# Kernel optimization log

Hardware: AMD Instinct MI355X
Metric: run time of the kernel (lower is better)

Reference implementation:

```python
import jax, jax.numpy as jnp
import numpy as np

DIM = 768
DEPTH = 12
HEADS = 12
DIM_HEAD = DIM // HEADS
DIM_MLP = 3072
PATCH = 16
SPECTRA = 4096
NUM_PATCHES = SPECTRA // PATCH
NUM_CLASSES = 1000
SCALE = DIM_HEAD ** -0.5
EPS = 1e-5


def sincos_pos_embed(embed_dim, n_pos):
    omega = np.arange(embed_dim // 2, dtype=np.float64) / (embed_dim / 2.0)
    omega = 1.0 / 10000 ** omega
    pos = np.arange(n_pos, dtype=np.float64)
    out = np.einsum('m,d->md', pos, omega)
    emb = np.concatenate([np.sin(out), np.cos(out)], axis=1)
    emb = np.concatenate([np.zeros([1, embed_dim]), emb], axis=0)  # cls slot
    return jnp.asarray(emb, jnp.float32)  # [N+1, D]


def setup_inputs() -> dict:
    key = jax.random.key(0)
    ks = jax.random.split(key, 12)
    s = 0.02
    d = {
        'x': jax.random.normal(ks[0], (32, 1, SPECTRA), jnp.float32),
        'conv_w': jax.random.normal(ks[1], (PATCH, DIM), jnp.float32) * s,
        'conv_b': jnp.zeros((DIM,), jnp.float32),
        'pos_embed': sincos_pos_embed(DIM, NUM_PATCHES),
        'cls_token': jax.random.normal(ks[2], (1, DIM), jnp.float32) * s,
        'ln1_w': jnp.ones((DEPTH, DIM), jnp.float32),
        'ln1_b': jnp.zeros((DEPTH, DIM), jnp.float32),
        'qkv_w': jax.random.normal(ks[3], (DEPTH, DIM, 3 * DIM), jnp.float32) * s,
        'out_w': jax.random.normal(ks[4], (DEPTH, DIM, DIM), jnp.float32) * s,
        'out_b': jnp.zeros((DEPTH, DIM), jnp.float32),
        'ln2_w': jnp.ones((DEPTH, DIM), jnp.float32),
        'ln2_b': jnp.zeros((DEPTH, DIM), jnp.float32),
        'mlp_w1': jax.random.normal(ks[5], (DEPTH, DIM, DIM_MLP), jnp.float32) * s,
        'mlp_b1': jnp.zeros((DEPTH, DIM_MLP), jnp.float32),
        'mlp_w2': jax.random.normal(ks[6], (DEPTH, DIM_MLP, DIM), jnp.float32) * s,
        'mlp_b2': jnp.zeros((DEPTH, DIM), jnp.float32),
        'cls_ln_w': jnp.ones((DIM,), jnp.float32),
        'cls_ln_b': jnp.zeros((DIM,), jnp.float32),
        'head_w': jax.random.normal(ks[7], (DIM, NUM_CLASSES), jnp.float32) * s,
        'head_b': jnp.zeros((NUM_CLASSES,), jnp.float32),
    }
    return d


def _ln(z, w, b):
    mu = z.mean(-1, keepdims=True)
    var = ((z - mu) ** 2).mean(-1, keepdims=True)
    return (z - mu) / jnp.sqrt(var + EPS) * w + b


def _forward(x, conv_w, conv_b, pos_embed, cls_token,
             ln1_w, ln1_b, qkv_w, out_w, out_b, ln2_w, ln2_b,
             mlp_w1, mlp_b1, mlp_w2, mlp_b2,
             cls_ln_w, cls_ln_b, head_w, head_b):
    B = x.shape[0]
    # Conv1d(1, D, k=P, stride=P) == non-overlapping patch linear proj
    patches = x.reshape(B, NUM_PATCHES, PATCH)
    h = patches @ conv_w + conv_b                         # [B, N, D]
    h = h + pos_embed[1:]
    cls = cls_token + pos_embed[:1]                       # [1, D]
    h = jnp.concatenate([jnp.broadcast_to(cls[None], (B, 1, DIM)), h], axis=1)  # [B, N+1, D]

    def block(h, p):
        l1w, l1b, qw, ow, ob, l2w, l2b, w1, b1, w2, b2 = p
        skip = h
        z = _ln(h, l1w, l1b)
        qkv = z @ qw                                      # [B, n, 3D]
        q, k, v = jnp.split(qkv, 3, axis=-1)
        def heads(t):
            return t.reshape(B, -1, HEADS, DIM_HEAD).transpose(0, 2, 1, 3)
        q, k, v = heads(q), heads(k), heads(v)            # [B, H, n, dh]
        dots = jnp.einsum('bhid,bhjd->bhij', q, k) * SCALE
        attn = jax.nn.softmax(dots, axis=-1)
        o = jnp.einsum('bhij,bhjd->bhid', attn, v)
        o = o.transpose(0, 2, 1, 3).reshape(B, -1, DIM)
        h = o @ ow + ob + skip
        skip = h
        z = _ln(h, l2w, l2b)
        z = jax.nn.gelu(z @ w1 + b1, approximate=False) @ w2 + b2
        return z + skip, None

    params = (ln1_w, ln1_b, qkv_w, out_w, out_b, ln2_w, ln2_b,
              mlp_w1, mlp_b1, mlp_w2, mlp_b2)
    h, _ = jax.lax.scan(block, h, params)
    cls_out = _ln(h[:, 0], cls_ln_w, cls_ln_b)
    return cls_out @ head_w + head_b                      # [B, num_classes]


def reference(x, conv_w, conv_b, pos_embed, cls_token,
              ln1_w, ln1_b, qkv_w, out_w, out_b, ln2_w, ln2_b,
              mlp_w1, mlp_b1, mlp_w2, mlp_b2,
              cls_ln_w, cls_ln_b, head_w, head_b):
    return _forward(x, conv_w, conv_b, pos_embed, cls_token,
                    ln1_w, ln1_b, qkv_w, out_w, out_b, ln2_w, ln2_b,
                    mlp_w1, mlp_b1, mlp_w2, mlp_b2,
                    cls_ln_w, cls_ln_b, head_w, head_b)
```

## Files before the change

### kernel.cpp

```cpp
#include <hip/hip_runtime.h>
#include <math.h>

#define DIM 768
#define DEPTH 12
#define HEADS 12
#define DIM_HEAD 64
#define DIM_MLP 3072
#define PATCH 16
#define NUM_PATCHES 256
#define SEQ 257
#define NUM_CLASSES 1000
#define BATCH 32
#define SCALE 0.125f
#define EPS 1e-5f
#define ROWS 8224
#define PAD_ROWS 8320
#define PAD_A 8448

typedef short bf16x8 __attribute__((ext_vector_type(8)));
typedef float f32x4 __attribute__((ext_vector_type(4)));

__device__ inline unsigned short f2bf(float f) {
    union { float f; unsigned int u; } c; c.f = f;
    unsigned int u = c.u;
    return (unsigned short)((u + 0x7fffu + ((u >> 16) & 1u)) >> 16);
}

#define MFMA16(d, a, b) d = __builtin_amdgcn_mfma_f32_16x16x32_bf16(a, b, d, 0, 0, 0)
#define SBAR() asm volatile("s_barrier" ::: "memory")
#define LGKM0() asm volatile("s_waitcnt lgkmcnt(0)" ::: "memory")

__global__ void patch_embed_kernel(const float* __restrict__ x,
                                   const float* __restrict__ conv_w,
                                   const float* __restrict__ conv_b,
                                   const float* __restrict__ pos,
                                   const float* __restrict__ cls_tok,
                                   float* __restrict__ h) {
    int row = blockIdx.x;
    int b = row / SEQ;
    int r = row % SEQ;
    int t = threadIdx.x;
    float* out = h + (long)row * DIM;
    if (r == 0) {
        for (int d = t; d < DIM; d += 256)
            out[d] = cls_tok[d] + pos[d];
        return;
    }
    int p = r - 1;
    const float* xp = x + (long)b * 4096 + p * PATCH;
    float xv[PATCH];
#pragma unroll
    for (int k = 0; k < PATCH; ++k) xv[k] = xp[k];
    for (int d = t; d < DIM; d += 256) {
        float acc = conv_b[d];
#pragma unroll
        for (int k = 0; k < PATCH; ++k)
            acc += xv[k] * conv_w[k * DIM + d];
        out[d] = acc + pos[(long)r * DIM + d];
    }
}

template <int OBF>
__global__ void layernorm_kernel(const float* __restrict__ in, long in_stride,
                                 const float* __restrict__ w,
                                 const float* __restrict__ bia,
                                 void* __restrict__ out) {
    __shared__ float red[8];
    long row = blockIdx.x;
    const float* src = in + row * in_stride;
    int t = threadIdx.x;
    float v0 = src[t], v1 = src[t + 256], v2 = src[t + 512];
    float s = v0 + v1 + v2;
    float q = v0 * v0 + v1 * v1 + v2 * v2;
#pragma unroll
    for (int off = 32; off; off >>= 1) {
        s += __shfl_down(s, off);
        q += __shfl_down(q, off);
    }
    if ((t & 63) == 0) { red[t >> 6] = s; red[4 + (t >> 6)] = q; }
    __syncthreads();
    if (t == 0) {
        float ss = red[0] + red[1] + red[2] + red[3];
        float qq = red[4] + red[5] + red[6] + red[7];
        float mu = ss * (1.0f / DIM);
        float var = qq * (1.0f / DIM) - mu * mu;
        red[0] = mu;
        red[1] = rsqrtf(var + EPS);
    }
    __syncthreads();
    float mu = red[0], rstd = red[1];
    float o0 = (v0 - mu) * rstd * w[t] + bia[t];
    float o1 = (v1 - mu) * rstd * w[t + 256] + bia[t + 256];
    float o2 = (v2 - mu) * rstd * w[t + 512] + bia[t + 512];
    if (OBF) {
        unsigned short* dst = (unsigned short*)out + row * DIM;
        dst[t] = f2bf(o0); dst[t + 256] = f2bf(o1); dst[t + 512] = f2bf(o2);
    } else {
        float* dst = (float*)out + row * DIM;
        dst[t] = o0; dst[t + 256] = o1; dst[t + 512] = o2;
    }
}

__global__ void transpose_all_kernel(const float* __restrict__ qw,
                                     const float* __restrict__ ow,
                                     const float* __restrict__ w1,
                                     const float* __restrict__ w2,
                                     unsigned short* __restrict__ qwT,
                                     unsigned short* __restrict__ owT,
                                     unsigned short* __restrict__ w1T,
                                     unsigned short* __restrict__ w2T) {
    __shared__ float tile[32][33];
    int t = blockIdx.x;
    const float* src; unsigned short* dst; int K, N, kt, nt;
    if (t < 1728)      {            src = qw; dst = qwT; K = 768;  N = 2304; kt = t % 24; nt = t / 24; }
    else if (t < 2304) { t -= 1728; src = ow; dst = owT; K = 768;  N = 768;  kt = t % 24; nt = t / 24; }
    else if (t < 4608) { t -= 2304; src = w1; dst = w1T; K = 768;  N = 3072; kt = t % 24; nt = t / 24; }
    else               { t -= 4608; src = w2; dst = w2T; K = 3072; N = 768;  kt = t % 96; nt = t / 96; }
    int k0 = kt * 32, n0 = nt * 32;
    int c = threadIdx.x & 31, r0 = threadIdx.x >> 5;
#pragma unroll
    for (int rr = r0; rr < 32; rr += 8)
        tile[rr][c] = src[(long)(k0 + rr) * N + n0 + c];
    __syncthreads();
#pragma unroll
    for (int rr = r0; rr < 32; rr += 8)
        dst[(long)(n0 + rr) * K + k0 + c] = f2bf(tile[c][rr]);
}

__global__ __launch_bounds__(256) void attn_kernel(const unsigned short* __restrict__ qkv,
                                                   unsigned short* __restrict__ o) {
    __shared__ unsigned short sh[60416];
    const int tid = threadIdx.x;
    const int lane = tid & 63;
    const int w = tid >> 6;

    const int nwg = gridDim.x;
    const int orig = blockIdx.x;
    const int q = nwg >> 3, r = nwg & 7;
    const int xcd = orig & 7, idx = orig >> 3;
    const int wg = (xcd < r ? xcd * (q + 1) : r * (q + 1) + (xcd - r) * q) + idx;
    const int bh = wg / 5, qt = wg % 5;
    const int b = bh / HEADS, hh = bh % HEADS;
    const unsigned short* qbase = qkv + (long)b * SEQ * 2304 + hh * 64;
    const unsigned short* kbase = qbase + 768;
    const unsigned short* vbase = qbase + 1536;

#pragma unroll
    for (int u = 0; u < 2; ++u) {
        int c = tid + u * 256;
        int j = c >> 3, cb = c & 7;
        int gj = qt * 64 + j; if (gj > 256) gj = 256;
        const unsigned short* g = qbase + (long)gj * 2304 + ((cb ^ (j & 7)) << 3);
        __builtin_amdgcn_global_load_lds(
            (const __attribute__((address_space(1))) void*)g,
            (__attribute__((address_space(3))) void*)&sh[j * 64 + cb * 8], 16, 0, 0);
    }
#pragma unroll
    for (int u = 0; u < 9; ++u) {
        int c = tid + u * 256;
        int j = c >> 3, cb = c & 7;
        int gj = j > 256 ? 256 : j;
        const unsigned short* g = kbase + (long)gj * 2304 + ((cb ^ (j & 7)) << 3);
        __builtin_amdgcn_global_load_lds(
            (const __attribute__((address_space(1))) void*)g,
            (__attribute__((address_space(3))) void*)&sh[4096 + j * 64 + cb * 8], 16, 0, 0);
    }
#pragma unroll
    for (int u = 0; u < 9; ++u) {
        int c = tid + u * 256;
        int j = c >> 3, dc = c & 7;
        short vv[8] = {0, 0, 0, 0, 0, 0, 0, 0};
        if (j < SEQ) *(bf16x8*)vv = *(const bf16x8*)(vbase + (long)j * 2304 + dc * 8);
#pragma unroll
        for (int e = 0; e < 8; ++e)
            sh[22528 + (dc * 8 + e) * 296 + j] = (unsigned short)vv[e];
    }
    __syncthreads();

    f32x4 s[18] = {};
#pragma unroll
    for (int ks = 0; ks < 2; ++ks) {
        int arow = w * 16 + (lane & 15);
        int cb = ks * 4 + (lane >> 4);
        bf16x8 aq = *(const bf16x8*)&sh[arow * 64 + ((cb ^ (arow & 7)) << 3)];
#pragma unroll
        for (int nf = 0; nf < 18; ++nf) {
            int brow = nf * 16 + (lane & 15);
            bf16x8 bk = *(const bf16x8*)&sh[4096 + brow * 64 + ((cb ^ (brow & 7)) << 3)];
            MFMA16(s[nf], aq, bk);
        }
    }

    float inv[4];
#pragma unroll
    for (int j = 0; j < 4; ++j) {
        float m_ = -3.0e38f;
#pragma unroll
        for (int nf = 0; nf < 18; ++nf) {
            int col = nf * 16 + (lane & 15);
            float x = (col < SEQ) ? s[nf][j] * SCALE : -3.0e38f;
            s[nf][j] = x;
            m_ = fmaxf(m_, x);
        }
#pragma unroll
        for (int off = 1; off < 16; off <<= 1) m_ = fmaxf(m_, __shfl_xor(m_, off));
        float sm = 0.f;
#pragma unroll
        for (int nf = 0; nf < 18; ++nf) {
            float e = __expf(s[nf][j] - m_);
            s[nf][j] = e;
            sm += e;
        }
#pragma unroll
        for (int off = 1; off < 16; off <<= 1) sm += __shfl_xor(sm, off);
        inv[j] = 1.0f / sm;
    }
#pragma unroll
    for (int nf = 0; nf < 18; ++nf) {
        int col = nf * 16 + (lane & 15);
#pragma unroll
        for (int j = 0; j < 4; ++j) {
            int row = w * 16 + (lane >> 4) * 4 + j;
            sh[41472 + row * 296 + col] = f2bf(s[nf][j] * inv[j]);
        }
    }
    __syncthreads();

    f32x4 oa[4] = {};
#pragma unroll
    for (int ks = 0; ks < 9; ++ks) {
        int prow = w * 16 + (lane & 15);
        bf16x8 ap = *(const bf16x8*)&sh[41472 + prow * 296 + ks * 32 + (lane >> 4) * 8];
#pragma unroll
        for (int n = 0; n < 4; ++n) {
            int drow = n * 16 + (lane & 15);
            bf16x8 bv = *(const bf16x8*)&sh[22528 + drow * 296 + ks * 32 + (lane >> 4) * 8];
            MFMA16(oa[n], ap, bv);
        }
    }
#pragma unroll
    for (int n = 0; n < 4; ++n) {
        int col = hh * 64 + n * 16 + (lane & 15);
#pragma unroll
        for (int j = 0; j < 4; ++j) {
            int gr = qt * 64 + w * 16 + (lane >> 4) * 4 + j;
            if (gr < SEQ)
                o[((long)(b * SEQ + gr)) * DIM + col] = f2bf(oa[n][j]);
        }
    }
}

template <int NK, int ACT>
__global__ __launch_bounds__(512, 2) void gemm256_kernel(
    const unsigned short* __restrict__ A,
    const unsigned short* __restrict__ Bt,
    const float* __restrict__ bias,
    unsigned short* __restrict__ C,
    int M, int GY, int lda, int ldb, int ldc) {
    __shared__ unsigned short sh[65536];
    const int tid = threadIdx.x;
    const int lane = tid & 63;
    const int w = tid >> 6;
    const int wr = w >> 2;
    const int wn = w & 3;

    const int nwg = gridDim.x;
    const int orig = blockIdx.x;
    const int q = nwg >> 3, r = nwg & 7;
    const int xcd = orig & 7, idx = orig >> 3;
    const int wg = (xcd < r ? xcd * (q + 1) : r * (q + 1) + (xcd - r) * q) + idx;
    const int bm = (wg / GY) * 256;
    const int bn = (wg % GY) * 256;

    const unsigned short* Ag = A + (long)bm * lda;
    const unsigned short* Bg = Bt + (long)bn * ldb;

    auto stageA = [&](int kt, int half) {
        unsigned short* Lb = &sh[(kt & 1) * 32768];
#pragma unroll
        for (int u = 0; u < 2; ++u) {
            int c = tid + u * 512;
            int lr = c >> 3, cb = c & 7;
            int row = ((lr >> 6) << 7) + (half << 6) + (lr & 63);
            const unsigned short* g = Ag + (long)row * lda + kt * 64 + ((cb ^ (row & 7)) << 3);
            __builtin_amdgcn_global_load_lds(
                (const __attribute__((address_space(1))) void*)g,
                (__attribute__((address_space(3))) void*)&Lb[row * 64 + (cb << 3)], 16, 0, 0);
        }
    };
    auto stageB = [&](int kt, int half) {
        unsigned short* Lb = &sh[(kt & 1) * 32768 + 16384];
#pragma unroll
        for (int u = 0; u < 2; ++u) {
            int c = tid + u * 512;
            int lr = c >> 3, cb = c & 7;
            int row = ((lr >> 5) << 6) + (half << 5) + (lr & 31);
            const unsigned short* g = Bg + (long)row * ldb + kt * 64 + ((cb ^ (row & 7)) << 3);
            __builtin_amdgcn_global_load_lds(
                (const __attribute__((address_space(1))) void*)g,
                (__attribute__((address_space(3))) void*)&Lb[row * 64 + (cb << 3)], 16, 0, 0);
        }
    };
    auto ldA = [&](int p, int m, int ks) {
        int row = wr * 128 + m * 16 + (lane & 15);
        int cb = ks * 4 + (lane >> 4);
        return *(const bf16x8*)&sh[p * 32768 + row * 64 + ((cb ^ (row & 7)) << 3)];
    };
    auto ldB = [&](int p, int n, int ks) {
        int row = wn * 64 + n * 16 + (lane & 15);
        int cb = ks * 4 + (lane >> 4);
        return *(const bf16x8*)&sh[p * 32768 + 16384 + row * 64 + ((cb ^ (row & 7)) << 3)];
    };

    f32x4 acc[8][4] = {};

    stageA(0, 0); stageA(0, 1); stageB(0, 0); stageB(0, 1);
    stageA(1, 0); stageA(1, 1); stageB(1, 0); stageB(1, 1);
    asm volatile("s_waitcnt vmcnt(8)" ::: "memory");
    SBAR();

    bf16x8 a[4][2], b01[2][2], b23[2][2];
    for (int kt = 0; kt < NK; ++kt) {
        const int p = kt & 1;
#pragma unroll
        for (int m = 0; m < 4; ++m) { a[m][0] = ldA(p, m, 0); a[m][1] = ldA(p, m, 1); }
#pragma unroll
        for (int n = 0; n < 2; ++n) { b01[n][0] = ldB(p, n, 0); b01[n][1] = ldB(p, n, 1); }
        SBAR(); LGKM0();
        __builtin_amdgcn_s_setprio(1);
#pragma unroll
        for (int m = 0; m < 4; ++m)
#pragma unroll
            for (int n = 0; n < 2; ++n) {
                MFMA16(acc[m][n], a[m][0], b01[n][0]);
                MFMA16(acc[m][n], a[m][1], b01[n][1]);
            }
        __builtin_amdgcn_s_setprio(0);
        SBAR();
#pragma unroll
        for (int n = 0; n < 2; ++n) { b23[n][0] = ldB(p, n + 2, 0); b23[n][1] = ldB(p, n + 2, 1); }
        if (kt + 2 < NK) stageA(kt + 2, 0);
        SBAR(); LGKM0();
        __builtin_amdgcn_s_setprio(1);
#pragma unroll
        for (int m = 0; m < 4; ++m)
#pragma unroll
            for (int n = 0; n < 2; ++n) {
                MFMA16(acc[m][n + 2], a[m][0], b23[n][0]);
                MFMA16(acc[m][n + 2], a[m][1], b23[n][1]);
            }
        __builtin_amdgcn_s_setprio(0);
        SBAR();
#pragma unroll
        for (int m = 0; m < 4; ++m) { a[m][0] = ldA(p, m + 4, 0); a[m][1] = ldA(p, m + 4, 1); }
        if (kt + 2 < NK) stageB(kt + 2, 0);
        SBAR(); LGKM0();
        __builtin_amdgcn_s_setprio(1);
#pragma unroll
        for (int m = 0; m < 4; ++m)
#pragma unroll
            for (int n = 0; n < 2; ++n) {
                MFMA16(acc[m + 4][n + 2], a[m][0], b23[n][0]);
                MFMA16(acc[m + 4][n + 2], a[m][1], b23[n][1]);
            }
        __builtin_amdgcn_s_setprio(0);
        SBAR();
        if (kt + 2 < NK) { stageA(kt + 2, 1); stageB(kt + 2, 1); }
        SBAR();
        __builtin_amdgcn_s_setprio(1);
#pragma unroll
        for (int m = 0; m < 4; ++m)
#pragma unroll
            for (int n = 0; n < 2; ++n) {
                MFMA16(acc[m + 4][n], a[m][0], b01[n][0]);
                MFMA16(acc[m + 4][n], a[m][1], b01[n][1]);
            }
        __builtin_amdgcn_s_setprio(0);
        if (kt + 2 < NK) {
            asm volatile("s_waitcnt vmcnt(8)" ::: "memory");
        } else if (kt + 1 < NK) {
            asm volatile("s_waitcnt vmcnt(0)" ::: "memory");
        }
        SBAR();
    }

#pragma unroll
    for (int mi = 0; mi < 8; ++mi) {
        int gr0 = bm + wr * 128 + mi * 16 + (lane >> 4) * 4;
#pragma unroll
        for (int ni = 0; ni < 4; ++ni) {
            int gc = bn + wn * 64 + ni * 16 + (lane & 15);
            float bv = bias ? bias[gc] : 0.f;
#pragma unroll
            for (int j = 0; j < 4; ++j) {
                int gr = gr0 + j;
                if (gr >= M) continue;
                float v = acc[mi][ni][j] + bv;
                if (ACT) v = 0.5f * v * (1.0f + erff(v * 0.70710678118654752f));
                C[(long)gr * ldc + gc] = f2bf(v);
            }
        }
    }
}

template <int NK, int ACT, int OBF>
__global__ __launch_bounds__(512, 2) void gemm8_kernel(
    const unsigned short* __restrict__ A,
    const unsigned short* __restrict__ Bt,
    const float* __restrict__ bias,
    const float* __restrict__ resid,
    void* __restrict__ C,
    int M, int GY, int lda, int ldb, int ldc) {
    __shared__ unsigned short sh[49152];
    const int tid = threadIdx.x;
    const int lane = tid & 63;
    const int w = tid >> 6;
    const int wr = w >> 2;
    const int wn = w & 3;

    const int nwg = gridDim.x;
    const int orig = blockIdx.x;
    const int q = nwg >> 3, r = nwg & 7;
    const int xcd = orig & 7, idx = orig >> 3;
    const int wg = (xcd < r ? xcd * (q + 1) : r * (q + 1) + (xcd - r) * q) + idx;
    const int bm = (wg / GY) * 128;
    const int bn = (wg % GY) * 256;

    const unsigned short* Ag = A + (long)bm * lda;
    const unsigned short* Bg = Bt + (long)bn * ldb;

    auto stageA = [&](int kt) {
        unsigned short* Lb = &sh[(kt & 1) * 24576];
#pragma unroll
        for (int u = 0; u < 2; ++u) {
            int c = tid + u * 512;
            int lr = c >> 3, cb = c & 7;
            const unsigned short* g = Ag + (long)lr * lda + kt * 64 + ((cb ^ (lr & 7)) << 3);
            __builtin_amdgcn_global_load_lds(
                (const __attribute__((address_space(1))) void*)g,
                (__attribute__((address_space(3))) void*)&Lb[lr * 64 + (cb << 3)], 16, 0, 0);
        }
    };
    auto stageB = [&](int kt, int half) {
        unsigned short* Lb = &sh[(kt & 1) * 24576 + 8192];
#pragma unroll
        for (int u = 0; u < 2; ++u) {
            int c = tid + u * 512;
            int lr = c >> 3, cb = c & 7;
            int br = ((lr >> 5) << 6) + (half << 5) + (lr & 31);
            const unsigned short* g = Bg + (long)br * ldb + kt * 64 + ((cb ^ (br & 7)) << 3);
            __builtin_amdgcn_global_load_lds(
                (const __attribute__((address_space(1))) void*)g,
                (__attribute__((address_space(3))) void*)&Lb[br * 64 + (cb << 3)], 16, 0, 0);
        }
    };
    auto ldA = [&](int p, int ms, int ks) {
        int row = wr * 64 + ms * 16 + (lane & 15);
        int cb = ks * 4 + (lane >> 4);
        return *(const bf16x8*)&sh[p * 24576 + row * 64 + ((cb ^ (row & 7)) << 3)];
    };
    auto ldB = [&](int p, int ns, int ks) {
        int br = wn * 64 + ns * 16 + (lane & 15);
        int cb = ks * 4 + (lane >> 4);
        return *(const bf16x8*)&sh[p * 24576 + 8192 + br * 64 + ((cb ^ (br & 7)) << 3)];
    };

    f32x4 acc[4][4] = {};

    stageB(0, 0); stageB(0, 1); stageA(0);
    stageB(1, 0); stageB(1, 1); stageA(1);
    asm volatile("s_waitcnt vmcnt(6)" ::: "memory");
    SBAR();

#pragma unroll 2
    for (int kt = 0; kt < NK; ++kt) {
        const int p = kt & 1;
        bf16x8 aA = ldA(p, 0, 0), aB = ldA(p, 0, 1), aC = ldA(p, 1, 0), aD = ldA(p, 1, 1);
        bf16x8 b0A = ldB(p, 0, 0), b0B = ldB(p, 0, 1), b0C = ldB(p, 1, 0), b0D = ldB(p, 1, 1);
        SBAR(); LGKM0();
        __builtin_amdgcn_s_setprio(1);
        MFMA16(acc[0][0], aA, b0A); MFMA16(acc[0][0], aB, b0B);
        MFMA16(acc[0][1], aA, b0C); MFMA16(acc[0][1], aB, b0D);
        MFMA16(acc[1][0], aC, b0A); MFMA16(acc[1][0], aD, b0B);
        MFMA16(acc[1][1], aC, b0C); MFMA16(acc[1][1], aD, b0D);
        __builtin_amdgcn_s_setprio(0);
        SBAR();
        bf16x8 b1A = ldB(p, 2, 0), b1B = ldB(p, 2, 1), b1C = ldB(p, 3, 0), b1D = ldB(p, 3, 1);
        if (kt + 2 < NK) stageB(kt + 2, 0);
        SBAR(); LGKM0();
        __builtin_amdgcn_s_setprio(1);
        MFMA16(acc[0][2], aA, b1A); MFMA16(acc[0][2], aB, b1B);
        MFMA16(acc[0][3], aA, b1C); MFMA16(acc[0][3], aB, b1D);
        MFMA16(acc[1][2], aC, b1A); MFMA16(acc[1][2], aD, b1B);
        MFMA16(acc[1][3], aC, b1C); MFMA16(acc[1][3], aD, b1D);
        __builtin_amdgcn_s_setprio(0);
        SBAR();
        aA = ldA(p, 2, 0); aB = ldA(p, 2, 1); aC = ldA(p, 3, 0); aD = ldA(p, 3, 1);
        if (kt + 2 < NK) stageB(kt + 2, 1);
        SBAR(); LGKM0();
        __builtin_amdgcn_s_setprio(1);
        MFMA16(acc[2][2], aA, b1A); MFMA16(acc[2][2], aB, b1B);
        MFMA16(acc[2][3], aA, b1C); MFMA16(acc[2][3], aB, b1D);
        MFMA16(acc[3][2], aC, b1A); MFMA16(acc[3][2], aD, b1B);
        MFMA16(acc[3][3], aC, b1C); MFMA16(acc[3][3], aD, b1D);
        __builtin_amdgcn_s_setprio(0);
        SBAR();
        if (kt + 2 < NK) stageA(kt + 2);
        SBAR();
        __builtin_amdgcn_s_setprio(1);
        MFMA16(acc[2][0], aA, b0A); MFMA16(acc[2][0], aB, b0B);
        MFMA16(acc[2][1], aA, b0C); MFMA16(acc[2][1], aB, b0D);
        MFMA16(acc[3][0], aC, b0A); MFMA16(acc[3][0], aD, b0B);
        MFMA16(acc[3][1], aC, b0C); MFMA16(acc[3][1], aD, b0D);
        __builtin_amdgcn_s_setprio(0);
        if (kt + 2 < NK) {
            asm volatile("s_waitcnt vmcnt(6)" ::: "memory");
        } else if (kt + 1 < NK) {
            asm volatile("s_waitcnt vmcnt(0)" ::: "memory");
        }
        SBAR();
    }

#pragma unroll
    for (int mi = 0; mi < 4; ++mi) {
        int gr0 = bm + wr * 64 + mi * 16 + (lane >> 4) * 4;
#pragma unroll
        for (int ni = 0; ni < 4; ++ni) {
            int gc = bn + wn * 64 + ni * 16 + (lane & 15);
            float bv = bias ? bias[gc] : 0.f;
#pragma unroll
            for (int j = 0; j < 4; ++j) {
                int gr = gr0 + j;
                if (gr >= M) continue;
                float v = acc[mi][ni][j] + bv;
                if (ACT) v = 0.5f * v * (1.0f + erff(v * 0.70710678118654752f));
                long ci = (long)gr * ldc + gc;
                if (OBF) {
                    ((unsigned short*)C)[ci] = f2bf(v);
                } else {
                    if (resid) v += resid[ci];
                    ((float*)C)[ci] = v;
                }
            }
        }
    }
}

__global__ void gemm_f32_kernel(const float* __restrict__ A,
                                const float* __restrict__ W,
                                const float* __restrict__ bias,
                                float* __restrict__ C,
                                int M, int N, int K) {
    __shared__ float As[16][65];
    __shared__ float Bs[16][65];
    int bm = blockIdx.x * 64, bn = blockIdx.y * 64;
    int t = threadIdx.x;
    int tx = t & 15, ty = t >> 4;
    float acc[4][4] = {};
    for (int k0 = 0; k0 < K; k0 += 16) {
        {
            int ar = bm + (t >> 2);
            int ac = k0 + (t & 3) * 4;
            float4 av = make_float4(0.f, 0.f, 0.f, 0.f);
            if (ar < M) av = *(const float4*)(A + (long)ar * K + ac);
            int kk = (t & 3) * 4, rr = t >> 2;
            As[kk + 0][rr] = av.x; As[kk + 1][rr] = av.y;
            As[kk + 2][rr] = av.z; As[kk + 3][rr] = av.w;
        }
        {
            int wr2 = k0 + (t >> 4);
            int wc2 = bn + (t & 15) * 4;
            float4 wv;
            wv.x = (wc2 + 0 < N) ? W[(long)wr2 * N + wc2 + 0] : 0.f;
            wv.y = (wc2 + 1 < N) ? W[(long)wr2 * N + wc2 + 1] : 0.f;
            wv.z = (wc2 + 2 < N) ? W[(long)wr2 * N + wc2 + 2] : 0.f;
            wv.w = (wc2 + 3 < N) ? W[(long)wr2 * N + wc2 + 3] : 0.f;
            int kr = t >> 4, nc = (t & 15) * 4;
            Bs[kr][nc + 0] = wv.x; Bs[kr][nc + 1] = wv.y;
            Bs[kr][nc + 2] = wv.z; Bs[kr][nc + 3] = wv.w;
        }
        __syncthreads();
#pragma unroll
        for (int kk = 0; kk < 16; ++kk) {
            float a0 = As[kk][ty * 4 + 0], a1 = As[kk][ty * 4 + 1];
            float a2 = As[kk][ty * 4 + 2], a3 = As[kk][ty * 4 + 3];
            float b0 = Bs[kk][tx], b1 = Bs[kk][tx + 16];
            float b2 = Bs[kk][tx + 32], b3 = Bs[kk][tx + 48];
            acc[0][0] += a0 * b0; acc[0][1] += a0 * b1; acc[0][2] += a0 * b2; acc[0][3] += a0 * b3;
            acc[1][0] += a1 * b0; acc[1][1] += a1 * b1; acc[1][2] += a1 * b2; acc[1][3] += a1 * b3;
            acc[2][0] += a2 * b0; acc[2][1] += a2 * b1; acc[2][2] += a2 * b2; acc[2][3] += a2 * b3;
            acc[3][0] += a3 * b0; acc[3][1] += a3 * b1; acc[3][2] += a3 * b2; acc[3][3] += a3 * b3;
        }
        __syncthreads();
    }
#pragma unroll
    for (int i = 0; i < 4; ++i) {
        int r = bm + ty * 4 + i;
        if (r >= M) continue;
#pragma unroll
        for (int j = 0; j < 4; ++j) {
            int c = bn + tx + 16 * j;
            if (c >= N) continue;
            C[(long)r * N + c] = acc[i][j] + (bias ? bias[c] : 0.f);
        }
    }
}

extern "C" void kernel_launch(void* const* d_in, const int* in_sizes, int n_in,
                              void* d_out, int out_size, void* d_ws, size_t ws_size,
                              hipStream_t stream) {
    const float* x        = (const float*)d_in[0];
    const float* conv_w   = (const float*)d_in[1];
    const float* conv_b   = (const float*)d_in[2];
    const float* pos      = (const float*)d_in[3];
    const float* cls_tok  = (const float*)d_in[4];
    const float* ln1_w    = (const float*)d_in[5];
    const float* ln1_b    = (const float*)d_in[6];
    const float* qkv_w    = (const float*)d_in[7];
    const float* out_w    = (const float*)d_in[8];
    const float* out_b    = (const float*)d_in[9];
    const float* ln2_w    = (const float*)d_in[10];
    const float* ln2_b    = (const float*)d_in[11];
    const float* mlp_w1   = (const float*)d_in[12];
    const float* mlp_b1   = (const float*)d_in[13];
    const float* mlp_w2   = (const float*)d_in[14];
    const float* mlp_b2   = (const float*)d_in[15];
    const float* cls_ln_w = (const float*)d_in[16];
    const float* cls_ln_b = (const float*)d_in[17];
    const float* head_w   = (const float*)d_in[18];
    const float* head_b   = (const float*)d_in[19];
    float* out = (float*)d_out;

    char* cur = (char*)d_ws;
    auto alloc = [&](size_t bytes) {
        void* p = cur; cur += (bytes + 255) & ~(size_t)255; return p;
    };
    float*          h      = (float*)alloc((size_t)PAD_ROWS * DIM * 4);
    unsigned short* z_bf   = (unsigned short*)alloc((size_t)PAD_A * DIM * 2);
    unsigned short* qkv_bf = (unsigned short*)alloc((size_t)ROWS * 3 * DIM * 2);
    unsigned short* o_bf   = (unsigned short*)alloc((size_t)PAD_ROWS * DIM * 2);
    unsigned short* m1     = (unsigned short*)alloc((size_t)PAD_ROWS * DIM_MLP * 2);
    unsigned short* qkvwT  = (unsigned short*)alloc((size_t)2304 * 768 * 2);
    unsigned short* owT    = (unsigned short*)alloc((size_t)768 * 768 * 2);
    unsigned short* w1T    = (unsigned short*)alloc((size_t)3072 * 768 * 2);
    unsigned short* w2T    = (unsigned short*)alloc((size_t)768 * 3072 * 2);
    float*          clsz   = (float*)alloc((size_t)BATCH * DIM * 4);

    patch_embed_kernel<<<ROWS, 256, 0, stream>>>(x, conv_w, conv_b, pos, cls_tok, h);

    for (int l = 0; l < DEPTH; ++l) {
        transpose_all_kernel<<<6912, 256, 0, stream>>>(
            qkv_w + (long)l * DIM * 3 * DIM, out_w + (long)l * DIM * DIM,
            mlp_w1 + (long)l * DIM * DIM_MLP, mlp_w2 + (long)l * DIM_MLP * DIM,
            qkvwT, owT, w1T, w2T);

        layernorm_kernel<1><<<ROWS, 256, 0, stream>>>(
            h, DIM, ln1_w + (long)l * DIM, ln1_b + (long)l * DIM, z_bf);

        gemm256_kernel<12, 0><<<33 * 9, 512, 0, stream>>>(
            z_bf, qkvwT, nullptr, qkv_bf, ROWS, 9, DIM, DIM, 3 * DIM);

        attn_kernel<<<384 * 5, 256, 0, stream>>>(qkv_bf, o_bf);

        gemm8_kernel<12, 0, 0><<<65 * 3, 512, 0, stream>>>(
            o_bf, owT, out_b + (long)l * DIM, h, h, ROWS, 3, DIM, DIM, DIM);

        layernorm_kernel<1><<<ROWS, 256, 0, stream>>>(
            h, DIM, ln2_w + (long)l * DIM, ln2_b + (long)l * DIM, z_bf);

        gemm256_kernel<12, 1><<<33 * 12, 512, 0, stream>>>(
            z_bf, w1T, mlp_b1 + (long)l * DIM_MLP, m1, ROWS, 12, DIM, DIM, DIM_MLP);

        gemm8_kernel<48, 0, 0><<<65 * 3, 512, 0, stream>>>(
            m1, w2T, mlp_b2 + (long)l * DIM, h, h, ROWS, 3, DIM_MLP, DIM_MLP, DIM);
    }

    layernorm_kernel<0><<<BATCH, 256, 0, stream>>>(
        h, (long)SEQ * DIM, cls_ln_w, cls_ln_b, clsz);
    gemm_f32_kernel<<<dim3(1, 16), 256, 0, stream>>>(
        clsz, head_w, head_b, out, BATCH, NUM_CLASSES, DIM);
}
```

Measured before the change: 4.625 ms.

## Replace 256x256 and 128x256 GEMMs with one 128x128 double-buffered kernel

Swaps the two 512-thread GEMM kernels (256x256 and 128x256 tiles, with staggered sub-stage pipelining) for a single 256-thread 128x128-tile kernel that stages A and B together. All four per-layer GEMMs now use it, with more workgroups per launch. The aim is better CU coverage and less tail waste, since the old grids of 297, 396 and 195 blocks fill the 256 CUs unevenly. The cost is lower arithmetic intensity per tile, more global/L2 traffic, and simpler pipelining with less overlap between loads and MFMA.

```diff
diff --git a/kernel.cpp b/kernel.cpp
--- a/kernel.cpp
+++ b/kernel.cpp
@@ -250,130 +250,83 @@
     }
 }
 
-template <int NK, int ACT>
-__global__ __launch_bounds__(512, 2) void gemm256_kernel(
+template <int NK, int ACT, int OBF>
+__global__ __launch_bounds__(256, 2) void gemmd_kernel(
     const unsigned short* __restrict__ A,
     const unsigned short* __restrict__ Bt,
     const float* __restrict__ bias,
-    unsigned short* __restrict__ C,
+    const float* __restrict__ resid,
+    void* __restrict__ C,
     int M, int GY, int lda, int ldb, int ldc) {
-    __shared__ unsigned short sh[65536];
+    __shared__ unsigned short sh[32768];
     const int tid = threadIdx.x;
     const int lane = tid & 63;
     const int w = tid >> 6;
-    const int wr = w >> 2;
-    const int wn = w & 3;
+    const int wr = w >> 1, wc = w & 1;
 
     const int nwg = gridDim.x;
     const int orig = blockIdx.x;
     const int q = nwg >> 3, r = nwg & 7;
     const int xcd = orig & 7, idx = orig >> 3;
     const int wg = (xcd < r ? xcd * (q + 1) : r * (q + 1) + (xcd - r) * q) + idx;
-    const int bm = (wg / GY) * 256;
-    const int bn = (wg % GY) * 256;
+    const int bm = (wg / GY) * 128;
+    const int bn = (wg % GY) * 128;
 
     const unsigned short* Ag = A + (long)bm * lda;
     const unsigned short* Bg = Bt + (long)bn * ldb;
 
-    auto stageA = [&](int kt, int half) {
-        unsigned short* Lb = &sh[(kt & 1) * 32768];
-#pragma unroll
-        for (int u = 0; u < 2; ++u) {
-            int c = tid + u * 512;
+    auto stage = [&](int kt) {
+        unsigned short* La = &sh[(kt & 1) * 16384];
+        unsigned short* Lb = La + 8192;
+#pragma unroll
+        for (int u = 0; u < 4; ++u) {
+            int c = tid + u * 256;
             int lr = c >> 3, cb = c & 7;
-            int row = ((lr >> 6) << 7) + (half << 6) + (lr & 63);
-            const unsigned short* g = Ag + (long)row * lda + kt * 64 + ((cb ^ (row & 7)) << 3);
+            int sw = (cb ^ (lr & 7)) << 3;
+            const unsigned short* ga = Ag + (long)lr * lda + kt * 64 + sw;
             __builtin_amdgcn_global_load_lds(
-                (const __attribute__((address_space(1))) void*)g,
-                (__attribute__((address_space(3))) void*)&Lb[row * 64 + (cb << 3)], 16, 0, 0);
-        }
-    };
-    auto stageB = [&](int kt, int half) {
-        unsigned short* Lb = &sh[(kt & 1) * 32768 + 16384];
-#pragma unroll
-        for (int u = 0; u < 2; ++u) {
-            int c = tid + u * 512;
-            int lr = c >> 3, cb = c & 7;
-            int row = ((lr >> 5) << 6) + (half << 5) + (lr & 31);
-            const unsigned short* g = Bg + (long)row * ldb + kt * 64 + ((cb ^ (row & 7)) << 3);
+                (const __attribute__((address_space(1))) void*)ga,
+                (__attribute__((address_space(3))) void*)&La[lr * 64 + (cb << 3)], 16, 0, 0);
+            const unsigned short* gb = Bg + (long)lr * ldb + kt * 64 + sw;
             __builtin_amdgcn_global_load_lds(
-                (const __attribute__((address_space(1))) void*)g,
-                (__attribute__((address_space(3))) void*)&Lb[row * 64 + (cb << 3)], 16, 0, 0);
+                (const __attribute__((address_space(1))) void*)gb,
+                (__attribute__((address_space(3))) void*)&Lb[lr * 64 + (cb << 3)], 16, 0, 0);
         }
     };
     auto ldA = [&](int p, int m, int ks) {
-        int row = wr * 128 + m * 16 + (lane & 15);
+        int row = wr * 64 + m * 16 + (lane & 15);
         int cb = ks * 4 + (lane >> 4);
-        return *(const bf16x8*)&sh[p * 32768 + row * 64 + ((cb ^ (row & 7)) << 3)];
+        return *(const bf16x8*)&sh[p * 16384 + row * 64 + ((cb ^ (row & 7)) << 3)];
     };
     auto ldB = [&](int p, int n, int ks) {
-        int row = wn * 64 + n * 16 + (lane & 15);
+        int row = wc * 64 + n * 16 + (lane & 15);
         int cb = ks * 4 + (lane >> 4);
-        return *(const bf16x8*)&sh[p * 32768 + 16384 + row * 64 + ((cb ^ (row & 7)) << 3)];
+        return *(const bf16x8*)&sh[p * 16384 + 8192 + row * 64 + ((cb ^ (row & 7)) << 3)];
     };
 
-    f32x4 acc[8][4] = {};
-
-    stageA(0, 0); stageA(0, 1); stageB(0, 0); stageB(0, 1);
-    stageA(1, 0); stageA(1, 1); stageB(1, 0); stageB(1, 1);
+    f32x4 acc[4][4] = {};
+
+    stage(0); stage(1);
     asm volatile("s_waitcnt vmcnt(8)" ::: "memory");
     SBAR();
 
-    bf16x8 a[4][2], b01[2][2], b23[2][2];
     for (int kt = 0; kt < NK; ++kt) {
         const int p = kt & 1;
+        bf16x8 a[4][2], b[4][2];
 #pragma unroll
         for (int m = 0; m < 4; ++m) { a[m][0] = ldA(p, m, 0); a[m][1] = ldA(p, m, 1); }
 #pragma unroll
-        for (int n = 0; n < 2; ++n) { b01[n][0] = ldB(p, n, 0); b01[n][1] = ldB(p, n, 1); }
-        SBAR(); LGKM0();
+        for (int n = 0; n < 4; ++n) { b[n][0] = ldB(p, n, 0); b[n][1] = ldB(p, n, 1); }
+        SBAR();
+        if (kt + 2 < NK) stage(kt + 2);
+        LGKM0();
         __builtin_amdgcn_s_setprio(1);
 #pragma unroll
         for (int m = 0; m < 4; ++m)
 #pragma unroll
-            for (int n = 0; n < 2; ++n) {
-                MFMA16(acc[m][n], a[m][0], b01[n][0]);
-                MFMA16(acc[m][n], a[m][1], b01[n][1]);
-            }
-        __builtin_amdgcn_s_setprio(0);
-        SBAR();
-#pragma unroll
-        for (int n = 0; n < 2; ++n) { b23[n][0] = ldB(p, n + 2, 0); b23[n][1] = ldB(p, n + 2, 1); }
-        if (kt + 2 < NK) stageA(kt + 2, 0);
-        SBAR(); LGKM0();
-        __builtin_amdgcn_s_setprio(1);
-#pragma unroll
-        for (int m = 0; m < 4; ++m)
-#pragma unroll
-            for (int n = 0; n < 2; ++n) {
-                MFMA16(acc[m][n + 2], a[m][0], b23[n][0]);
-                MFMA16(acc[m][n + 2], a[m][1], b23[n][1]);
-            }
-        __builtin_amdgcn_s_setprio(0);
-        SBAR();
-#pragma unroll
-        for (int m = 0; m < 4; ++m) { a[m][0] = ldA(p, m + 4, 0); a[m][1] = ldA(p, m + 4, 1); }
-        if (kt + 2 < NK) stageB(kt + 2, 0);
-        SBAR(); LGKM0();
-        __builtin_amdgcn_s_setprio(1);
-#pragma unroll
-        for (int m = 0; m < 4; ++m)
-#pragma unroll
-            for (int n = 0; n < 2; ++n) {
-                MFMA16(acc[m + 4][n + 2], a[m][0], b23[n][0]);
-                MFMA16(acc[m + 4][n + 2], a[m][1], b23[n][1]);
-            }
-        __builtin_amdgcn_s_setprio(0);
-        SBAR();
-        if (kt + 2 < NK) { stageA(kt + 2, 1); stageB(kt + 2, 1); }
-        SBAR();
-        __builtin_amdgcn_s_setprio(1);
-#pragma unroll
-        for (int m = 0; m < 4; ++m)
-#pragma unroll
-            for (int n = 0; n < 2; ++n) {
-                MFMA16(acc[m + 4][n], a[m][0], b01[n][0]);
-                MFMA16(acc[m + 4][n], a[m][1], b01[n][1]);
+            for (int n = 0; n < 4; ++n) {
+                MFMA16(acc[m][n], a[m][0], b[n][0]);
+                MFMA16(acc[m][n], a[m][1], b[n][1]);
             }
         __builtin_amdgcn_s_setprio(0);
         if (kt + 2 < NK) {
@@ -385,148 +338,11 @@
     }
 
 #pragma unroll
-    for (int mi = 0; mi < 8; ++mi) {
-        int gr0 = bm + wr * 128 + mi * 16 + (lane >> 4) * 4;
-#pragma unroll
-        for (int ni = 0; ni < 4; ++ni) {
-            int gc = bn + wn * 64 + ni * 16 + (lane & 15);
-            float bv = bias ? bias[gc] : 0.f;
-#pragma unroll
-            for (int j = 0; j < 4; ++j) {
-                int gr = gr0 + j;
-                if (gr >= M) continue;
-                float v = acc[mi][ni][j] + bv;
-                if (ACT) v = 0.5f * v * (1.0f + erff(v * 0.70710678118654752f));
-                C[(long)gr * ldc + gc] = f2bf(v);
-            }
-        }
-    }
-}
-
-template <int NK, int ACT, int OBF>
-__global__ __launch_bounds__(512, 2) void gemm8_kernel(
-    const unsigned short* __restrict__ A,
-    const unsigned short* __restrict__ Bt,
-    const float* __restrict__ bias,
-    const float* __restrict__ resid,
-    void* __restrict__ C,
-    int M, int GY, int lda, int ldb, int ldc) {
-    __shared__ unsigned short sh[49152];
-    const int tid = threadIdx.x;
-    const int lane = tid & 63;
-    const int w = tid >> 6;
-    const int wr = w >> 2;
-    const int wn = w & 3;
-
-    const int nwg = gridDim.x;
-    const int orig = blockIdx.x;
-    const int q = nwg >> 3, r = nwg & 7;
-    const int xcd = orig & 7, idx = orig >> 3;
-    const int wg = (xcd < r ? xcd * (q + 1) : r * (q + 1) + (xcd - r) * q) + idx;
-    const int bm = (wg / GY) * 128;
-    const int bn = (wg % GY) * 256;
-
-    const unsigned short* Ag = A + (long)bm * lda;
-    const unsigned short* Bg = Bt + (long)bn * ldb;
-
-    auto stageA = [&](int kt) {
-        unsigned short* Lb = &sh[(kt & 1) * 24576];
-#pragma unroll
-        for (int u = 0; u < 2; ++u) {
-            int c = tid + u * 512;
-            int lr = c >> 3, cb = c & 7;
-            const unsigned short* g = Ag + (long)lr * lda + kt * 64 + ((cb ^ (lr & 7)) << 3);
-            __builtin_amdgcn_global_load_lds(
-                (const __attribute__((address_space(1))) void*)g,
-                (__attribute__((address_space(3))) void*)&Lb[lr * 64 + (cb << 3)], 16, 0, 0);
-        }
-    };
-    auto stageB = [&](int kt, int half) {
-        unsigned short* Lb = &sh[(kt & 1) * 24576 + 8192];
-#pragma unroll
-        for (int u = 0; u < 2; ++u) {
-            int c = tid + u * 512;
-            int lr = c >> 3, cb = c & 7;
-            int br = ((lr >> 5) << 6) + (half << 5) + (lr & 31);
-            const unsigned short* g = Bg + (long)br * ldb + kt * 64 + ((cb ^ (br & 7)) << 3);
-            __builtin_amdgcn_global_load_lds(
-                (const __attribute__((address_space(1))) void*)g,
-                (__attribute__((address_space(3))) void*)&Lb[br * 64 + (cb << 3)], 16, 0, 0);
-        }
-    };
-    auto ldA = [&](int p, int ms, int ks) {
-        int row = wr * 64 + ms * 16 + (lane & 15);
-        int cb = ks * 4 + (lane >> 4);
-        return *(const bf16x8*)&sh[p * 24576 + row * 64 + ((cb ^ (row & 7)) << 3)];
-    };
-    auto ldB = [&](int p, int ns, int ks) {
-        int br = wn * 64 + ns * 16 + (lane & 15);
-        int cb = ks * 4 + (lane >> 4);
-        return *(const bf16x8*)&sh[p * 24576 + 8192 + br * 64 + ((cb ^ (br & 7)) << 3)];
-    };
-
-    f32x4 acc[4][4] = {};
-
-    stageB(0, 0); stageB(0, 1); stageA(0);
-    stageB(1, 0); stageB(1, 1); stageA(1);
-    asm volatile("s_waitcnt vmcnt(6)" ::: "memory");
-    SBAR();
-
-#pragma unroll 2
-    for (int kt = 0; kt < NK; ++kt) {
-        const int p = kt & 1;
-        bf16x8 aA = ldA(p, 0, 0), aB = ldA(p, 0, 1), aC = ldA(p, 1, 0), aD = ldA(p, 1, 1);
-        bf16x8 b0A = ldB(p, 0, 0), b0B = ldB(p, 0, 1), b0C = ldB(p, 1, 0), b0D = ldB(p, 1, 1);
-        SBAR(); LGKM0();
-        __builtin_amdgcn_s_setprio(1);
-        MFMA16(acc[0][0], aA, b0A); MFMA16(acc[0][0], aB, b0B);
-        MFMA16(acc[0][1], aA, b0C); MFMA16(acc[0][1], aB, b0D);
-        MFMA16(acc[1][0], aC, b0A); MFMA16(acc[1][0], aD, b0B);
-        MFMA16(acc[1][1], aC, b0C); MFMA16(acc[1][1], aD, b0D);
-        __builtin_amdgcn_s_setprio(0);
-        SBAR();
-        bf16x8 b1A = ldB(p, 2, 0), b1B = ldB(p, 2, 1), b1C = ldB(p, 3, 0), b1D = ldB(p, 3, 1);
-        if (kt + 2 < NK) stageB(kt + 2, 0);
-        SBAR(); LGKM0();
-        __builtin_amdgcn_s_setprio(1);
-        MFMA16(acc[0][2], aA, b1A); MFMA16(acc[0][2], aB, b1B);
-        MFMA16(acc[0][3], aA, b1C); MFMA16(acc[0][3], aB, b1D);
-        MFMA16(acc[1][2], aC, b1A); MFMA16(acc[1][2], aD, b1B);
-        MFMA16(acc[1][3], aC, b1C); MFMA16(acc[1][3], aD, b1D);
-        __builtin_amdgcn_s_setprio(0);
-        SBAR();
-        aA = ldA(p, 2, 0); aB = ldA(p, 2, 1); aC = ldA(p, 3, 0); aD = ldA(p, 3, 1);
-        if (kt + 2 < NK) stageB(kt + 2, 1);
-        SBAR(); LGKM0();
-        __builtin_amdgcn_s_setprio(1);
-        MFMA16(acc[2][2], aA, b1A); MFMA16(acc[2][2], aB, b1B);
-        MFMA16(acc[2][3], aA, b1C); MFMA16(acc[2][3], aB, b1D);
-        MFMA16(acc[3][2], aC, b1A); MFMA16(acc[3][2], aD, b1B);
-        MFMA16(acc[3][3], aC, b1C); MFMA16(acc[3][3], aD, b1D);
-        __builtin_amdgcn_s_setprio(0);
-        SBAR();
-        if (kt + 2 < NK) stageA(kt + 2);
-        SBAR();
-        __builtin_amdgcn_s_setprio(1);
-        MFMA16(acc[2][0], aA, b0A); MFMA16(acc[2][0], aB, b0B);
-        MFMA16(acc[2][1], aA, b0C); MFMA16(acc[2][1], aB, b0D);
-        MFMA16(acc[3][0], aC, b0A); MFMA16(acc[3][0], aD, b0B);
-        MFMA16(acc[3][1], aC, b0C); MFMA16(acc[3][1], aD, b0D);
-        __builtin_amdgcn_s_setprio(0);
-        if (kt + 2 < NK) {
-            asm volatile("s_waitcnt vmcnt(6)" ::: "memory");
-        } else if (kt + 1 < NK) {
-            asm volatile("s_waitcnt vmcnt(0)" ::: "memory");
-        }
-        SBAR();
-    }
-
-#pragma unroll
     for (int mi = 0; mi < 4; ++mi) {
         int gr0 = bm + wr * 64 + mi * 16 + (lane >> 4) * 4;
 #pragma unroll
         for (int ni = 0; ni < 4; ++ni) {
-            int gc = bn + wn * 64 + ni * 16 + (lane & 15);
+            int gc = bn + wc * 64 + ni * 16 + (lane & 15);
             float bv = bias ? bias[gc] : 0.f;
 #pragma unroll
             for (int j = 0; j < 4; ++j) {
@@ -657,22 +473,22 @@
         layernorm_kernel<1><<<ROWS, 256, 0, stream>>>(
             h, DIM, ln1_w + (long)l * DIM, ln1_b + (long)l * DIM, z_bf);
 
-        gemm256_kernel<12, 0><<<33 * 9, 512, 0, stream>>>(
-            z_bf, qkvwT, nullptr, qkv_bf, ROWS, 9, DIM, DIM, 3 * DIM);
+        gemmd_kernel<12, 0, 1><<<65 * 18, 256, 0, stream>>>(
+            z_bf, qkvwT, nullptr, nullptr, qkv_bf, ROWS, 18, DIM, DIM, 3 * DIM);
 
         attn_kernel<<<384 * 5, 256, 0, stream>>>(qkv_bf, o_bf);
 
-        gemm8_kernel<12, 0, 0><<<65 * 3, 512, 0, stream>>>(
-            o_bf, owT, out_b + (long)l * DIM, h, h, ROWS, 3, DIM, DIM, DIM);
+        gemmd_kernel<12, 0, 0><<<65 * 6, 256, 0, stream>>>(
+            o_bf, owT, out_b + (long)l * DIM, h, h, ROWS, 6, DIM, DIM, DIM);
 
         layernorm_kernel<1><<<ROWS, 256, 0, stream>>>(
             h, DIM, ln2_w + (long)l * DIM, ln2_b + (long)l * DIM, z_bf);
 
-        gemm256_kernel<12, 1><<<33 * 12, 512, 0, stream>>>(
-            z_bf, w1T, mlp_b1 + (long)l * DIM_MLP, m1, ROWS, 12, DIM, DIM, DIM_MLP);
-
-        gemm8_kernel<48, 0, 0><<<65 * 3, 512, 0, stream>>>(
-            m1, w2T, mlp_b2 + (long)l * DIM, h, h, ROWS, 3, DIM_MLP, DIM_MLP, DIM);
+        gemmd_kernel<12, 1, 1><<<65 * 24, 256, 0, stream>>>(
+            z_bf, w1T, mlp_b1 + (long)l * DIM_MLP, nullptr, m1, ROWS, 24, DIM, DIM, DIM_MLP);
+
+        gemmd_kernel<48, 0, 0><<<65 * 6, 256, 0, stream>>>(
+            m1, w2T, mlp_b2 + (long)l * DIM, h, h, ROWS, 6, DIM_MLP, DIM_MLP, DIM);
     }
 
     layernorm_kernel<0><<<BATCH, 256, 0, stream>>>(
```

Measured after the change: 4.404 ms. 1.05x faster.
